# Kernel optimization log

Measured on AMD Instinct MI355X. Metric: run time of the kernel, lower is better.

Reference implementation:

```python
import jax, jax.numpy as jnp
import numpy as np

HIDDEN = 2048
N_HEADS = 16
HEAD_DIM = HIDDEN // N_HEADS          # 128
KV_CHANNELS = 512
N_KV_HEADS = HIDDEN // KV_CHANNELS    # 4
ROTARY_BASE = 10000.0
ROTARY_DIM = HEAD_DIM                 # rotary_pct = 1.0
SCALE = HEAD_DIM ** -0.5
NEG = -1e9


def setup_inputs() -> dict:
    key = jax.random.key(0)
    k1, k2, k3 = jax.random.split(key, 3)
    B, S = 1, 2048
    hidden_states = jax.random.normal(k1, (B, S, HIDDEN), dtype=jnp.float32)
    # additive causal mask [B,1,S,S]
    causal = jnp.tril(jnp.ones((S, S), dtype=jnp.bool_))
    attention_mask = jnp.where(causal, 0.0, NEG).astype(jnp.float32)[None, None]
    position_ids = jnp.arange(S, dtype=jnp.int64 if jax.config.jax_enable_x64 else jnp.int32)[None].repeat(B, axis=0)
    # torch nn.Linear(in,out) stored as [in,out] so y = x @ W (no bias: no_bias=True)
    qkv_out = N_HEADS * HEAD_DIM + 2 * N_KV_HEADS * HEAD_DIM  # 3072
    W_attn = jax.random.normal(k2, (HIDDEN, qkv_out), dtype=jnp.float32) * (HIDDEN ** -0.5)
    W_proj = jax.random.normal(k3, (HIDDEN, HIDDEN), dtype=jnp.float32) * (HIDDEN ** -0.5)
    return {"hidden_states": hidden_states, "attention_mask": attention_mask,
            "position_ids": position_ids, "W_attn": W_attn, "W_proj": W_proj}


def _rotate_half(x):
    x1, x2 = jnp.split(x, 2, axis=-1)
    return jnp.concatenate([-x2, x1], axis=-1)


def _rope(q, k, position_ids):
    # Faithful to the source: emb = cat(sin(freqs), cos(freqs)); then use cos(emb), sin(emb)
    inv_freq = 1.0 / (ROTARY_BASE ** (jnp.arange(0, ROTARY_DIM, 2, dtype=jnp.float32) / ROTARY_DIM))
    t = position_ids.astype(jnp.float32)                      # [B,S]
    freqs = t[..., None] * inv_freq[None, None, :]            # [B,S,rd/2]
    emb = jnp.concatenate([jnp.sin(freqs), jnp.cos(freqs)], axis=-1)  # [B,S,rd]
    cos_e = jnp.cos(emb)[:, None, :, :]                       # [B,1,S,rd]
    sin_e = jnp.sin(emb)[:, None, :, :]
    q = q * cos_e + _rotate_half(q) * sin_e
    k = k * cos_e + _rotate_half(k) * sin_e
    return q, k


def reference(hidden_states, attention_mask, position_ids, W_attn, W_proj):
    B, S, _ = hidden_states.shape
    qkv = hidden_states @ W_attn                              # [B,S,3072]
    q_len = N_HEADS * HEAD_DIM
    kv_len = N_KV_HEADS * HEAD_DIM
    q, k, v = jnp.split(qkv, [q_len, q_len + kv_len], axis=-1)
    q = q.reshape(B, S, N_HEADS, HEAD_DIM).transpose(0, 2, 1, 3)      # [B,H,S,D]
    k = k.reshape(B, S, N_KV_HEADS, HEAD_DIM).transpose(0, 2, 1, 3)   # [B,Hkv,S,D]
    v = v.reshape(B, S, N_KV_HEADS, HEAD_DIM).transpose(0, 2, 1, 3)
    q, k = _rope(q, k, position_ids)
    # GQA: repeat_interleave over head dim
    rep = N_HEADS // N_KV_HEADS
    k = jnp.repeat(k, rep, axis=1)                            # [B,H,S,D]
    v = jnp.repeat(v, rep, axis=1)
    scores = jnp.einsum('bhqd,bhkd->bhqk', q, k) * SCALE + attention_mask
    probs = jax.nn.softmax(scores, axis=-1)
    attn = jnp.einsum('bhqk,bhkd->bhqd', probs, v)            # [B,H,S,D]
    attn = attn.transpose(0, 2, 1, 3).reshape(B, S, HIDDEN)
    return attn @ W_proj
```

## Files before the change

### kernel.cpp

```cpp
#include <hip/hip_runtime.h>


typedef short s16x8 __attribute__((ext_vector_type(8)));
typedef short s16x4 __attribute__((ext_vector_type(4)));
typedef float f32x4 __attribute__((ext_vector_type(4)));

#define MFMA16 __builtin_amdgcn_mfma_f32_16x16x32_bf16

static constexpr int S = 2048;
static constexpr int HID = 2048;
static constexpr int NH = 16;
static constexpr int HD = 128;
static constexpr int NKV = 4;
static constexpr int QKVN = 3072;
static constexpr float QSCALE = 0.12751743f;

__device__ __forceinline__ short f2bf(float f) {
  unsigned u = __float_as_uint(f);
  unsigned r = (u + 0x7FFFu + ((u >> 16) & 1u)) >> 16;
  return (short)r;
}
__device__ __forceinline__ float bf2f(short s) {
  return __uint_as_float(((unsigned)(unsigned short)s) << 16);
}
__device__ __forceinline__ void gload_lds16(const void* g, void* l) {
  __builtin_amdgcn_global_load_lds(
      (const __attribute__((address_space(1))) unsigned int*)g,
      (__attribute__((address_space(3))) unsigned int*)l, 16, 0, 0);
}

__global__ __launch_bounds__(256) void prep_kernel(
    const float* __restrict__ hidden, const float* __restrict__ Wa,
    const float* __restrict__ Wp, short* __restrict__ hid_bf,
    short* __restrict__ wat, short* __restrict__ wpt) {
  int b = blockIdx.x;
  if (b < 4096) {
    int i = (b * 256 + threadIdx.x) * 4;
    float4 v = *(const float4*)(hidden + i);
    s16x4 o;
    o[0] = f2bf(v.x); o[1] = f2bf(v.y); o[2] = f2bf(v.z); o[3] = f2bf(v.w);
    *(s16x4*)(hid_bf + i) = o;
    return;
  }
  __shared__ float tile[32][33];
  const float* W; short* Wt; int C, bx, by;
  if (b < 10240) {
    W = Wa; Wt = wat; C = QKVN;
    int u = b - 4096; bx = u % 96; by = u / 96;
  } else {
    W = Wp; Wt = wpt; C = HID;
    int u = b - 10240; bx = u & 63; by = u >> 6;
  }
  int c0 = bx * 32, r0 = by * 32;
  int tx = threadIdx.x & 31, ty = threadIdx.x >> 5;
#pragma unroll
  for (int j = 0; j < 4; j++)
    tile[ty + j * 8][tx] = W[(size_t)(r0 + ty + j * 8) * C + c0 + tx];
  __syncthreads();
#pragma unroll
  for (int j = 0; j < 4; j++)
    Wt[(size_t)(c0 + ty + j * 8) * HID + r0 + tx] = f2bf(tile[tx][ty + j * 8]);
}

__global__ __launch_bounds__(256) void ropevt_kernel(
    const short* __restrict__ qkv, short* __restrict__ Qb,
    short* __restrict__ Kb, short* __restrict__ Vt) {
  int b = blockIdx.x;
  if (b < 2048) {
    int s = b;
    float p = (float)s;
    const short* row = qkv + (size_t)s * QKVN;
#pragma unroll
    for (int j = 0; j < 5; j++) {
      int w = j * 256 + threadIdx.x;
      int hh = w >> 6, i = w & 63;
      float fr = p * __powf(10000.0f, -(float)i / 64.0f);
      float e1 = sinf(fr), e2 = cosf(fr);
      float c1 = cosf(e1), s1 = sinf(e1);
      float c2 = cosf(e2), s2 = sinf(e2);
      if (hh < NH) {
        const short* q = row + hh * HD;
        float a = bf2f(q[i]), bb = bf2f(q[i + 64]);
        Qb[((size_t)hh * S + s) * HD + i] = f2bf((a * c1 - bb * s1) * QSCALE);
        Qb[((size_t)hh * S + s) * HD + i + 64] =
            f2bf((bb * c2 + a * s2) * QSCALE);
      } else {
        int hk = hh - NH;
        const short* k = row + HID + hk * HD;
        float a = bf2f(k[i]), bb = bf2f(k[i + 64]);
        Kb[((size_t)hk * S + s) * HD + i] = f2bf(a * c1 - bb * s1);
        Kb[((size_t)hk * S + s) * HD + i + 64] = f2bf(bb * c2 + a * s2);
      }
    }
    return;
  }
  __shared__ short tile[32][34];
  int u = b - 2048;
  int s0 = (u & 63) * 32, d0 = ((u >> 6) & 3) * 32, hk = u >> 8;
  int tx = threadIdx.x & 31, ty = threadIdx.x >> 5;
#pragma unroll
  for (int j = 0; j < 4; j++)
    tile[ty + j * 8][tx] =
        qkv[(size_t)(s0 + ty + j * 8) * QKVN + 2560 + hk * 128 + d0 + tx];
  __syncthreads();
#pragma unroll
  for (int j = 0; j < 4; j++)
    Vt[((size_t)hk * HD + d0 + ty + j * 8) * S + s0 + tx] = tile[tx][ty + j * 8];
}

template <bool BF16OUT>
__global__ __launch_bounds__(256) void gemm_bt_kernel(
    const short* __restrict__ A, const short* __restrict__ Bt,
    void* __restrict__ Cout, int M, int N, int K) {
  __shared__ short As[2][4096];
  __shared__ short Bs[2][2048];
  int tid = threadIdx.x;
  int lane = tid & 63, wid = tid >> 6;
  int wr = wid >> 1, wc = wid & 1;
  int bm = blockIdx.y * 128, bn = blockIdx.x * 64;
  int srow = tid >> 2;
  int scol = (tid & 3) * 8;
  int rr = lane & 15;
  int kk = (lane >> 4) * 8;

  const short* Ag = A + (size_t)(bm + srow) * K + scol;
  const short* Bg = Bt + (size_t)(bn + srow) * K + scol;
  int ldst = wid * 512;

  f32x4 acc[4][2] = {};

  gload_lds16(Ag, &As[0][ldst]);
  gload_lds16(Ag + (size_t)64 * K, &As[0][ldst + 2048]);
  gload_lds16(Bg, &Bs[0][ldst]);
  Ag += 32; Bg += 32;
  asm volatile("s_waitcnt vmcnt(0)" ::: "memory");
  __syncthreads();

  int nk = K >> 5;
  for (int i = 0; i < nk; ++i) {
    int buf = i & 1;
    if (i + 1 < nk) {
      gload_lds16(Ag, &As[buf ^ 1][ldst]);
      gload_lds16(Ag + (size_t)64 * K, &As[buf ^ 1][ldst + 2048]);
      gload_lds16(Bg, &Bs[buf ^ 1][ldst]);
      Ag += 32; Bg += 32;
    }
    s16x8 af[4], bfr[2];
#pragma unroll
    for (int m = 0; m < 4; m++)
      af[m] = *(const s16x8*)&As[buf][(wr * 64 + m * 16 + rr) * 32 + kk];
#pragma unroll
    for (int n = 0; n < 2; n++)
      bfr[n] = *(const s16x8*)&Bs[buf][(wc * 32 + n * 16 + rr) * 32 + kk];
    __builtin_amdgcn_s_setprio(1);
#pragma unroll
    for (int m = 0; m < 4; m++)
#pragma unroll
      for (int n = 0; n < 2; n++)
        acc[m][n] = MFMA16(af[m], bfr[n], acc[m][n], 0, 0, 0);
    __builtin_amdgcn_s_setprio(0);
    asm volatile("s_waitcnt vmcnt(0)" ::: "memory");
    __syncthreads();
  }

  int crow0 = bm + wr * 64 + (lane >> 4) * 4;
  int ccol0 = bn + wc * 32 + rr;
#pragma unroll
  for (int m = 0; m < 4; m++)
#pragma unroll
    for (int n = 0; n < 2; n++)
#pragma unroll
      for (int r = 0; r < 4; r++) {
        size_t idx = (size_t)(crow0 + m * 16 + r) * N + ccol0 + n * 16;
        if (BF16OUT) ((short*)Cout)[idx] = f2bf(acc[m][n][r]);
        else ((float*)Cout)[idx] = acc[m][n][r];
      }
}

__global__ __launch_bounds__(256) void attn_kernel(
    const short* __restrict__ Q, const short* __restrict__ K,
    const short* __restrict__ Vt, short* __restrict__ Ob) {
  __shared__ short Ks[2][8192];
  __shared__ short Vs[2][8192];
  __shared__ short Pl[4][16][72];
  int wid = threadIdx.x >> 6, lane = threadIdx.x & 63;
  int gid = blockIdx.x;
  int u = gid >> 1;
  int h = u & 15;
  int v = u >> 4;
  int qb = (gid & 1) ? v : 31 - v;
  int hk = h >> 2;
  int q0 = qb * 64 + wid * 16;
  int rr = lane & 15, rg = lane >> 4, r7 = rr & 7;

  const short* Qh = Q + ((size_t)h * S + q0) * HD;
  s16x8 qf[4];
#pragma unroll
  for (int kc = 0; kc < 4; kc++)
    qf[kc] = *(const s16x8*)(Qh + rr * HD + kc * 32 + rg * 8);

  const short* Kh = K + (size_t)hk * S * HD;
  const short* Vh = Vt + (size_t)hk * HD * S;

  size_t koff[4], voff[4];
  int kdst[4], vdst[4];
#pragma unroll
  for (int g = 0; g < 4; g++) {
    int kr = wid * 16 + g * 4 + (lane >> 4);
    koff[g] = (size_t)kr * 128 + 8 * ((lane & 15) ^ (kr & 7));
    kdst[g] = (wid * 16 + g * 4) * 128;
    int vr = wid * 32 + g * 8 + (lane >> 3);
    voff[g] = (size_t)vr * S + 8 * ((lane & 7) ^ (vr & 7));
    vdst[g] = (wid * 32 + g * 8) * 64;
  }

  f32x4 o[8] = {};
  float mrow[4], plr[4];
#pragma unroll
  for (int r = 0; r < 4; r++) { mrow[r] = -1e30f; plr[r] = 0.0f; }

#pragma unroll
  for (int g = 0; g < 4; g++) {
    gload_lds16(Kh + koff[g], &Ks[0][kdst[g]]);
    gload_lds16(Vh + voff[g], &Vs[0][vdst[g]]);
  }
  asm volatile("s_waitcnt vmcnt(0)" ::: "memory");
  __syncthreads();

  for (int t = 0; t <= qb; ++t) {
    int buf = t & 1;
    if (t < qb) {
      size_t kvs = (size_t)(t + 1) * 64;
#pragma unroll
      for (int g = 0; g < 4; g++) {
        gload_lds16(Kh + kvs * 128 + koff[g], &Ks[buf ^ 1][kdst[g]]);
        gload_lds16(Vh + kvs + voff[g], &Vs[buf ^ 1][vdst[g]]);
      }
    }
    int kvb = t * 64;
    const short* Kb_ = Ks[buf];
    const short* Vb_ = Vs[buf];

    f32x4 sc4[4];
    __builtin_amdgcn_s_setprio(1);
#pragma unroll
    for (int c = 0; c < 4; c++) {
      f32x4 sacc = {};
#pragma unroll
      for (int kc = 0; kc < 4; kc++) {
        int chunk = (rg + kc * 4) ^ r7;
        s16x8 kf = *(const s16x8*)(Kb_ + (c * 16 + rr) * 128 + chunk * 8);
        sacc = MFMA16(qf[kc], kf, sacc, 0, 0, 0);
      }
      sc4[c] = sacc;
    }
    __builtin_amdgcn_s_setprio(0);

#pragma unroll
    for (int r = 0; r < 4; r++) {
      float v0 = sc4[0][r], v1 = sc4[1][r];
      float v2 = sc4[2][r], v3 = sc4[3][r];
      if (t == qb) {
        int qrow = q0 + rg * 4 + r;
        v0 += (kvb + rr) > qrow ? -1e9f : 0.0f;
        v1 += (kvb + 16 + rr) > qrow ? -1e9f : 0.0f;
        v2 += (kvb + 32 + rr) > qrow ? -1e9f : 0.0f;
        v3 += (kvb + 48 + rr) > qrow ? -1e9f : 0.0f;
      }
      float pmax = fmaxf(fmaxf(v0, v1), fmaxf(v2, v3));
      unsigned long long bal = __ballot(pmax > mrow[r] + 11.5f);
      if ((bal >> (rg * 16)) & 0xFFFFull) {
        float mx = pmax;
#pragma unroll
        for (int d = 1; d < 16; d <<= 1) mx = fmaxf(mx, __shfl_xor(mx, d, 64));
        float mn = fmaxf(mrow[r], mx);
        float scl = exp2f(mrow[r] - mn);
        mrow[r] = mn;
        plr[r] *= scl;
#pragma unroll
        for (int dc = 0; dc < 8; dc++) o[dc][r] *= scl;
      }
      float p0 = exp2f(v0 - mrow[r]), p1 = exp2f(v1 - mrow[r]);
      float p2 = exp2f(v2 - mrow[r]), p3 = exp2f(v3 - mrow[r]);
      plr[r] += (p0 + p1) + (p2 + p3);
      Pl[wid][rg * 4 + r][rr] = f2bf(p0);
      Pl[wid][rg * 4 + r][rr + 16] = f2bf(p1);
      Pl[wid][rg * 4 + r][rr + 32] = f2bf(p2);
      Pl[wid][rg * 4 + r][rr + 48] = f2bf(p3);
    }
    asm volatile("s_waitcnt lgkmcnt(0)" ::: "memory");
    __builtin_amdgcn_sched_barrier(0);
    s16x8 pf0 = *(const s16x8*)&Pl[wid][rr][rg * 8];
    s16x8 pf1 = *(const s16x8*)&Pl[wid][rr][32 + rg * 8];

    __builtin_amdgcn_s_setprio(1);
#pragma unroll
    for (int dc = 0; dc < 8; dc++) {
      int ch0 = rg ^ r7, ch1 = (rg + 4) ^ r7;
      s16x8 vf0 = *(const s16x8*)(Vb_ + (dc * 16 + rr) * 64 + ch0 * 8);
      s16x8 vf1 = *(const s16x8*)(Vb_ + (dc * 16 + rr) * 64 + ch1 * 8);
      o[dc] = MFMA16(pf0, vf0, o[dc], 0, 0, 0);
      o[dc] = MFMA16(pf1, vf1, o[dc], 0, 0, 0);
    }
    __builtin_amdgcn_s_setprio(0);

    asm volatile("s_waitcnt vmcnt(0)" ::: "memory");
    __syncthreads();
  }

#pragma unroll
  for (int r = 0; r < 4; r++) {
    float l = plr[r];
#pragma unroll
    for (int d = 1; d < 16; d <<= 1) l += __shfl_xor(l, d, 64);
    float inv = 1.0f / l;
    int srow = q0 + rg * 4 + r;
#pragma unroll
    for (int dc = 0; dc < 8; dc++)
      Ob[(size_t)srow * HID + h * HD + dc * 16 + rr] = f2bf(o[dc][r] * inv);
  }
}

extern "C" void kernel_launch(void* const* d_in, const int* in_sizes, int n_in,
                              void* d_out, int out_size, void* d_ws,
                              size_t ws_size, hipStream_t stream) {
  (void)in_sizes; (void)n_in; (void)out_size; (void)ws_size;
  const float* hidden = (const float*)d_in[0];
  const float* W_attn = (const float*)d_in[3];
  const float* W_proj = (const float*)d_in[4];
  float* out = (float*)d_out;

  char* ws = (char*)d_ws;
  short* hid_bf = (short*)(ws);
  short* wat    = (short*)(ws + 8388608);
  short* wpt    = (short*)(ws + 20971520);
  short* qkvb   = (short*)(ws + 29360128);
  short* Qb     = (short*)(ws + 41943040);
  short* Kb     = (short*)(ws + 50331648);
  short* Vt     = (short*)(ws + 52428800);
  short* Ab     = (short*)(ws + 54525952);

  hipLaunchKernelGGL(prep_kernel, dim3(14336), dim3(256), 0, stream,
                     hidden, W_attn, W_proj, hid_bf, wat, wpt);
  hipLaunchKernelGGL((gemm_bt_kernel<true>), dim3(QKVN / 64, S / 128),
                     dim3(256), 0, stream, hid_bf, wat, (void*)qkvb, S, QKVN,
                     HID);
  hipLaunchKernelGGL(ropevt_kernel, dim3(3072), dim3(256), 0, stream,
                     qkvb, Qb, Kb, Vt);
  hipLaunchKernelGGL(attn_kernel, dim3(512), dim3(256), 0, stream,
                     Qb, Kb, Vt, Ab);
  hipLaunchKernelGGL((gemm_bt_kernel<false>), dim3(HID / 64, S / 128),
                     dim3(256), 0, stream, Ab, wpt, (void*)out, S, HID, HID);
}
```

Before: 276.0 us.

## Triple-buffer GEMM loads, widen weight transpose tiles, reorder attention block mapping

The GEMM main loop moves from double to triple buffering with a prefetch distance of two and partial vmcnt waits, so global-to-LDS loads overlap more with MFMA work. The weight transpose in prep now uses 64x32 tiles, which halves the block count and lets each write row cover 64 contiguous bf16 elements. The attention grid is remapped so the first 256 blocks take the long causal query blocks and the second 256 take the short ones, in place of interleaving them. These trade extra LDS per GEMM block for deeper prefetch and may change occupancy and load balance.

Measured after the change: 273.9 us. About the same (-0.8%).

```diff
diff --git a/kernel.cpp b/kernel.cpp
--- a/kernel.cpp
+++ b/kernel.cpp
@@ -42,24 +42,25 @@
     *(s16x4*)(hid_bf + i) = o;
     return;
   }
-  __shared__ float tile[32][33];
+  __shared__ float tile[64][33];
   const float* W; short* Wt; int C, bx, by;
-  if (b < 10240) {
+  if (b < 7168) {
     W = Wa; Wt = wat; C = QKVN;
     int u = b - 4096; bx = u % 96; by = u / 96;
   } else {
     W = Wp; Wt = wpt; C = HID;
-    int u = b - 10240; bx = u & 63; by = u >> 6;
-  }
-  int c0 = bx * 32, r0 = by * 32;
+    int u = b - 7168; bx = u & 63; by = u >> 6;
+  }
+  int c0 = bx * 32, r0 = by * 64;
   int tx = threadIdx.x & 31, ty = threadIdx.x >> 5;
 #pragma unroll
-  for (int j = 0; j < 4; j++)
+  for (int j = 0; j < 8; j++)
     tile[ty + j * 8][tx] = W[(size_t)(r0 + ty + j * 8) * C + c0 + tx];
   __syncthreads();
-#pragma unroll
-  for (int j = 0; j < 4; j++)
-    Wt[(size_t)(c0 + ty + j * 8) * HID + r0 + tx] = f2bf(tile[tx][ty + j * 8]);
+  int tz = threadIdx.x & 63, tw = threadIdx.x >> 6;
+#pragma unroll
+  for (int j = 0; j < 8; j++)
+    Wt[(size_t)(c0 + tw * 8 + j) * HID + r0 + tz] = f2bf(tile[tz][tw * 8 + j]);
 }
 
 __global__ __launch_bounds__(256) void ropevt_kernel(
@@ -112,8 +113,8 @@
 __global__ __launch_bounds__(256) void gemm_bt_kernel(
     const short* __restrict__ A, const short* __restrict__ Bt,
     void* __restrict__ Cout, int M, int N, int K) {
-  __shared__ short As[2][4096];
-  __shared__ short Bs[2][2048];
+  __shared__ short As[3][4096];
+  __shared__ short Bs[3][2048];
   int tid = threadIdx.x;
   int lane = tid & 63, wid = tid >> 6;
   int wr = wid >> 1, wc = wid & 1;
@@ -133,25 +134,30 @@
   gload_lds16(Ag + (size_t)64 * K, &As[0][ldst + 2048]);
   gload_lds16(Bg, &Bs[0][ldst]);
   Ag += 32; Bg += 32;
-  asm volatile("s_waitcnt vmcnt(0)" ::: "memory");
-  __syncthreads();
+  gload_lds16(Ag, &As[1][ldst]);
+  gload_lds16(Ag + (size_t)64 * K, &As[1][ldst + 2048]);
+  gload_lds16(Bg, &Bs[1][ldst]);
+  Ag += 32; Bg += 32;
+  asm volatile("s_waitcnt vmcnt(3)" ::: "memory");
+  __builtin_amdgcn_sched_barrier(0);
+  __builtin_amdgcn_s_barrier();
 
   int nk = K >> 5;
+  int bcur = 0, bpre = 2;
   for (int i = 0; i < nk; ++i) {
-    int buf = i & 1;
-    if (i + 1 < nk) {
-      gload_lds16(Ag, &As[buf ^ 1][ldst]);
-      gload_lds16(Ag + (size_t)64 * K, &As[buf ^ 1][ldst + 2048]);
-      gload_lds16(Bg, &Bs[buf ^ 1][ldst]);
+    if (i + 2 < nk) {
+      gload_lds16(Ag, &As[bpre][ldst]);
+      gload_lds16(Ag + (size_t)64 * K, &As[bpre][ldst + 2048]);
+      gload_lds16(Bg, &Bs[bpre][ldst]);
       Ag += 32; Bg += 32;
     }
     s16x8 af[4], bfr[2];
 #pragma unroll
     for (int m = 0; m < 4; m++)
-      af[m] = *(const s16x8*)&As[buf][(wr * 64 + m * 16 + rr) * 32 + kk];
+      af[m] = *(const s16x8*)&As[bcur][(wr * 64 + m * 16 + rr) * 32 + kk];
 #pragma unroll
     for (int n = 0; n < 2; n++)
-      bfr[n] = *(const s16x8*)&Bs[buf][(wc * 32 + n * 16 + rr) * 32 + kk];
+      bfr[n] = *(const s16x8*)&Bs[bcur][(wc * 32 + n * 16 + rr) * 32 + kk];
     __builtin_amdgcn_s_setprio(1);
 #pragma unroll
     for (int m = 0; m < 4; m++)
@@ -159,8 +165,15 @@
       for (int n = 0; n < 2; n++)
         acc[m][n] = MFMA16(af[m], bfr[n], acc[m][n], 0, 0, 0);
     __builtin_amdgcn_s_setprio(0);
-    asm volatile("s_waitcnt vmcnt(0)" ::: "memory");
-    __syncthreads();
+    if (i + 2 < nk)
+      asm volatile("s_waitcnt vmcnt(3)" ::: "memory");
+    else
+      asm volatile("s_waitcnt vmcnt(0)" ::: "memory");
+    __builtin_amdgcn_sched_barrier(0);
+    __builtin_amdgcn_s_barrier();
+    __builtin_amdgcn_sched_barrier(0);
+    bcur = (bcur == 2) ? 0 : bcur + 1;
+    bpre = (bpre == 2) ? 0 : bpre + 1;
   }
 
   int crow0 = bm + wr * 64 + (lane >> 4) * 4;
@@ -185,10 +198,10 @@
   __shared__ short Pl[4][16][72];
   int wid = threadIdx.x >> 6, lane = threadIdx.x & 63;
   int gid = blockIdx.x;
-  int u = gid >> 1;
-  int h = u & 15;
-  int v = u >> 4;
-  int qb = (gid & 1) ? v : 31 - v;
+  int g = gid & 255;
+  int h = g & 15;
+  int v = (g >> 4) & 15;
+  int qb = (gid < 256) ? 31 - v : v;
   int hk = h >> 2;
   int q0 = qb * 64 + wid * 16;
   int rr = lane & 15, rg = lane >> 4, r7 = rr & 7;
@@ -205,13 +218,13 @@
   size_t koff[4], voff[4];
   int kdst[4], vdst[4];
 #pragma unroll
-  for (int g = 0; g < 4; g++) {
-    int kr = wid * 16 + g * 4 + (lane >> 4);
-    koff[g] = (size_t)kr * 128 + 8 * ((lane & 15) ^ (kr & 7));
-    kdst[g] = (wid * 16 + g * 4) * 128;
-    int vr = wid * 32 + g * 8 + (lane >> 3);
-    voff[g] = (size_t)vr * S + 8 * ((lane & 7) ^ (vr & 7));
-    vdst[g] = (wid * 32 + g * 8) * 64;
+  for (int g2 = 0; g2 < 4; g2++) {
+    int kr = wid * 16 + g2 * 4 + (lane >> 4);
+    koff[g2] = (size_t)kr * 128 + 8 * ((lane & 15) ^ (kr & 7));
+    kdst[g2] = (wid * 16 + g2 * 4) * 128;
+    int vr = wid * 32 + g2 * 8 + (lane >> 3);
+    voff[g2] = (size_t)vr * S + 8 * ((lane & 7) ^ (vr & 7));
+    vdst[g2] = (wid * 32 + g2 * 8) * 64;
   }
 
   f32x4 o[8] = {};
@@ -220,9 +233,9 @@
   for (int r = 0; r < 4; r++) { mrow[r] = -1e30f; plr[r] = 0.0f; }
 
 #pragma unroll
-  for (int g = 0; g < 4; g++) {
-    gload_lds16(Kh + koff[g], &Ks[0][kdst[g]]);
-    gload_lds16(Vh + voff[g], &Vs[0][vdst[g]]);
+  for (int g2 = 0; g2 < 4; g2++) {
+    gload_lds16(Kh + koff[g2], &Ks[0][kdst[g2]]);
+    gload_lds16(Vh + voff[g2], &Vs[0][vdst[g2]]);
   }
   asm volatile("s_waitcnt vmcnt(0)" ::: "memory");
   __syncthreads();
@@ -232,9 +245,9 @@
     if (t < qb) {
       size_t kvs = (size_t)(t + 1) * 64;
 #pragma unroll
-      for (int g = 0; g < 4; g++) {
-        gload_lds16(Kh + kvs * 128 + koff[g], &Ks[buf ^ 1][kdst[g]]);
-        gload_lds16(Vh + kvs + voff[g], &Vs[buf ^ 1][vdst[g]]);
+      for (int g2 = 0; g2 < 4; g2++) {
+        gload_lds16(Kh + kvs * 128 + koff[g2], &Ks[buf ^ 1][kdst[g2]]);
+        gload_lds16(Vh + kvs + voff[g2], &Vs[buf ^ 1][vdst[g2]]);
       }
     }
     int kvb = t * 64;
@@ -340,7 +353,7 @@
   short* Vt     = (short*)(ws + 52428800);
   short* Ab     = (short*)(ws + 54525952);
 
-  hipLaunchKernelGGL(prep_kernel, dim3(14336), dim3(256), 0, stream,
+  hipLaunchKernelGGL(prep_kernel, dim3(9216), dim3(256), 0, stream,
                      hidden, W_attn, W_proj, hid_bf, wat, wpt);
   hipLaunchKernelGGL((gemm_bt_kernel<true>), dim3(QKVN / 64, S / 128),
                      dim3(256), 0, stream, hid_bf, wat, (void*)qkvb, S, QKVN,
```
